# Kernel optimization log

Hardware: AMD Instinct MI355X
Metric: run time of the kernel (lower is better)

The kernel has to match this reference:

```python
import jax, jax.numpy as jnp
import numpy as np

B, T, D, H = 2, 2048, 2048, 16
HD = D // H
EPS = 1e-8
NEG = -1e9


def setup_inputs() -> dict:
    key = jax.random.key(0)
    ks = jax.random.split(key, 6)
    x = jax.random.normal(ks[0], (B, T, D), dtype=jnp.float32)
    # additive causal mask, broadcast over [B, H, T, T]
    causal = jnp.tril(jnp.ones((T, T), dtype=bool))
    attn_mask = jnp.where(causal, 0.0, NEG).astype(jnp.float32)[None, None]
    s = 1.0 / np.sqrt(D)
    w_norm = jnp.ones((D,), dtype=jnp.float32)
    wq = jax.random.normal(ks[1], (D, D), dtype=jnp.float32) * s
    wk = jax.random.normal(ks[2], (D, D), dtype=jnp.float32) * s
    wv = jax.random.normal(ks[3], (D, D), dtype=jnp.float32) * s
    wo = jax.random.normal(ks[4], (D, D), dtype=jnp.float32) * s
    return {"x": x, "attn_mask": attn_mask, "w_norm": w_norm,
            "wq": wq, "wk": wk, "wv": wv, "wo": wo}


def _rmsnorm(x, w):
    # norm = ||x||_2 * D^-0.5 ; out = w * x / (norm + eps)  (eps outside, as in source)
    norm = jnp.sqrt(jnp.sum(x * x, axis=-1, keepdims=True)) * (x.shape[-1] ** -0.5)
    return w * x / (norm + EPS)


def reference(x, attn_mask, w_norm, wq, wk, wv, wo):
    b, t, d = x.shape
    xn = _rmsnorm(x, w_norm)
    # Linear (no bias): y = x @ W^T ; split into heads -> [B, H, T, HD]
    def proj(w):
        return jnp.einsum('btd,ed->bte', xn, w).reshape(b, t, H, HD).transpose(0, 2, 1, 3)
    q, k, v = proj(wq), proj(wk), proj(wv)
    scale = HD ** -0.5
    w_scores = jnp.einsum('bhqd,bhkd->bhqk', q, k) * scale + attn_mask
    p = jax.nn.softmax(w_scores, axis=-1)
    out = jnp.einsum('bhqk,bhkd->bhqd', p, v)
    out = out.transpose(0, 2, 1, 3).reshape(b, t, d)
    return jnp.einsum('btd,ed->bte', out, wo)
```

## Files before the change

### kernel.cpp

```cpp
#include <hip/hip_runtime.h>
#include <stdint.h>

#define TT 2048
#define DD 2048
#define NHH 16
#define HDD 128
#define BTT 4096

typedef __attribute__((ext_vector_type(8))) short bf16x8;
typedef __attribute__((ext_vector_type(4))) float f32x4;

#define MF(a, b, c) __builtin_amdgcn_mfma_f32_16x16x32_bf16(a, b, c, 0, 0, 0)

__device__ __forceinline__ unsigned short f2bf(float f) {
    union { float f; uint32_t u; } v; v.f = f;
    uint32_t u = v.u;
    u += 0x7fffu + ((u >> 16) & 1u);
    return (unsigned short)(u >> 16);
}

__device__ __forceinline__ void gld16(const unsigned short* g, unsigned short* l) {
    __builtin_amdgcn_global_load_lds(
        (const __attribute__((address_space(1))) unsigned int*)g,
        (__attribute__((address_space(3))) unsigned int*)l, 16, 0, 0);
}

__global__ __launch_bounds__(256) void convert_w(const float* __restrict__ wq,
                                                 const float* __restrict__ wk,
                                                 const float* __restrict__ wv,
                                                 const float* __restrict__ wo,
                                                 unsigned short* __restrict__ out) {
    size_t gid = (size_t)blockIdx.x * 256 + threadIdx.x;
    size_t base = gid * 8;
    int which = (int)(base >> 22);
    const float* src = which == 0 ? wq : which == 1 ? wk : which == 2 ? wv : wo;
    size_t off = base & 4194303u;
    float4 a = ((const float4*)(src + off))[0];
    float4 b = ((const float4*)(src + off))[1];
    union { unsigned short us[8]; uint4 v; } pk;
    pk.us[0] = f2bf(a.x); pk.us[1] = f2bf(a.y); pk.us[2] = f2bf(a.z); pk.us[3] = f2bf(a.w);
    pk.us[4] = f2bf(b.x); pk.us[5] = f2bf(b.y); pk.us[6] = f2bf(b.z); pk.us[7] = f2bf(b.w);
    *(uint4*)(out + base) = pk.v;
}

__global__ __launch_bounds__(256) void rmsnorm_k(const float* __restrict__ x,
                                                 const float* __restrict__ w,
                                                 unsigned short* __restrict__ xn) {
    const int row = blockIdx.x;
    const int tid = threadIdx.x;
    const float* xr = x + (size_t)row * DD;
    float4 a = ((const float4*)xr)[tid * 2];
    float4 b = ((const float4*)xr)[tid * 2 + 1];
    float ss = a.x*a.x + a.y*a.y + a.z*a.z + a.w*a.w
             + b.x*b.x + b.y*b.y + b.z*b.z + b.w*b.w;
    #pragma unroll
    for (int m = 1; m < 64; m <<= 1) ss += __shfl_xor(ss, m, 64);
    __shared__ float wss[4];
    if ((tid & 63) == 0) wss[tid >> 6] = ss;
    __syncthreads();
    float total = wss[0] + wss[1] + wss[2] + wss[3];
    float norm = sqrtf(total) * 0.022097086912079612f;
    float inv = 1.0f / (norm + 1e-8f);
    float4 wa = ((const float4*)w)[tid * 2];
    float4 wb = ((const float4*)w)[tid * 2 + 1];
    union { unsigned short us[8]; uint4 v; } pk;
    pk.us[0] = f2bf(wa.x * a.x * inv); pk.us[1] = f2bf(wa.y * a.y * inv);
    pk.us[2] = f2bf(wa.z * a.z * inv); pk.us[3] = f2bf(wa.w * a.w * inv);
    pk.us[4] = f2bf(wb.x * b.x * inv); pk.us[5] = f2bf(wb.y * b.y * inv);
    pk.us[6] = f2bf(wb.z * b.z * inv); pk.us[7] = f2bf(wb.w * b.w * inv);
    ((uint4*)(xn + (size_t)row * DD))[tid] = pk.v;
}

__device__ __forceinline__ void gemm128x256_core(const unsigned short* __restrict__ Ag,
                                                 const unsigned short* __restrict__ Bg,
                                                 unsigned short* lds, f32x4 acc[4][4]) {
    const int tid = threadIdx.x;
    const int wave = tid >> 6, lane = tid & 63;
    const int wm = wave >> 2, wn = wave & 3;
    const int l15 = lane & 15, lq = lane >> 4;
    const unsigned short* ga  = Ag + (size_t)(wave * 16 + l15) * DD + lq * 8;
    const unsigned short* gb0 = Bg + (size_t)(wave * 32 + l15) * DD + lq * 8;
    const unsigned short* gb1 = Bg + (size_t)(wave * 32 + 16 + l15) * DD + lq * 8;
    const int da  = wave * 512 + lane * 8;
    const int db0 = 4096 + wave * 1024 + lane * 8;
    const int db1 = 4096 + wave * 1024 + 512 + lane * 8;
    const int ra = (wm * 4) * 512 + lq * 128 + l15 * 8;
    const int rb = 4096 + (wn * 4) * 512 + lq * 128 + l15 * 8;

    uint4 sA  = *(const uint4*)(ga);
    uint4 sB0 = *(const uint4*)(gb0);
    uint4 sB1 = *(const uint4*)(gb1);
    *(uint4*)(lds + da)  = sA;
    *(uint4*)(lds + db0) = sB0;
    *(uint4*)(lds + db1) = sB1;
    asm volatile("s_waitcnt lgkmcnt(0)" ::: "memory");
    __builtin_amdgcn_s_barrier();

    for (int kt = 0; kt < 64; kt++) {
        const int cur = (kt & 1) ? 12288 : 0;
        const int nxt = 12288 - cur;
        if (kt + 1 < 64) {
            const int ko = (kt + 1) * 32;
            sA  = *(const uint4*)(ga + ko);
            sB0 = *(const uint4*)(gb0 + ko);
            sB1 = *(const uint4*)(gb1 + ko);
            __builtin_amdgcn_sched_barrier(0);
        }
        const unsigned short* ac = lds + cur + ra;
        const unsigned short* bc = lds + cur + rb;
        bf16x8 a[4], b[4];
        #pragma unroll
        for (int i = 0; i < 4; i++) a[i] = *(const bf16x8*)(ac + i * 512);
        #pragma unroll
        for (int n = 0; n < 4; n++) b[n] = *(const bf16x8*)(bc + n * 512);
        asm volatile("s_waitcnt lgkmcnt(0)" ::: "memory");
        __builtin_amdgcn_sched_barrier(0);
        __builtin_amdgcn_s_setprio(1);
        #pragma unroll
        for (int i = 0; i < 4; i++)
            #pragma unroll
            for (int n = 0; n < 4; n++)
                acc[i][n] = MF(a[i], b[n], acc[i][n]);
        __builtin_amdgcn_s_setprio(0);
        if (kt + 1 < 64) {
            *(uint4*)(lds + nxt + da)  = sA;
            *(uint4*)(lds + nxt + db0) = sB0;
            *(uint4*)(lds + nxt + db1) = sB1;
            asm volatile("s_waitcnt lgkmcnt(0)" ::: "memory");
            __builtin_amdgcn_sched_barrier(0);
        }
        __builtin_amdgcn_s_barrier();
    }
}

__global__ __launch_bounds__(512, 4) void gemm_qkv(const unsigned short* __restrict__ A,
                                                   const unsigned short* __restrict__ W3,
                                                   unsigned short* __restrict__ O3) {
    __shared__ __align__(16) unsigned short lds[24576];
    const int orig = blockIdx.y * 32 + blockIdx.x;
    const int id = (orig & 7) * 96 + (orig >> 3);
    const int which = id >> 8;
    const int rem = id & 255;
    const int bn = rem >> 5, bm = rem & 31;
    const unsigned short* Bw = W3 + (size_t)which * DD * DD;
    unsigned short* C = O3 + (size_t)which * BTT * DD;
    const int m0 = bm * 128, n0 = bn * 256;
    const f32x4 zf = {0.f, 0.f, 0.f, 0.f};
    f32x4 acc[4][4];
    #pragma unroll
    for (int m = 0; m < 4; m++)
        #pragma unroll
        for (int n = 0; n < 4; n++) acc[m][n] = zf;
    gemm128x256_core(A + (size_t)m0 * DD, Bw + (size_t)n0 * DD, lds, acc);
    const int wave = threadIdx.x >> 6, lane = threadIdx.x & 63;
    const int wm = wave >> 2, wn = wave & 3;
    const int l15 = lane & 15, lq = lane >> 4;
    #pragma unroll
    for (int m = 0; m < 4; m++) {
        const int row = m0 + wm * 64 + m * 16 + lq * 4;
        #pragma unroll
        for (int n = 0; n < 4; n++) {
            const int col = n0 + wn * 64 + n * 16 + l15;
            #pragma unroll
            for (int r = 0; r < 4; r++)
                C[(size_t)(row + r) * DD + col] = f2bf(acc[m][n][r]);
        }
    }
}

__global__ __launch_bounds__(512, 4) void gemm_out(const unsigned short* __restrict__ A,
                                                   const unsigned short* __restrict__ Bw,
                                                   float* __restrict__ C) {
    __shared__ __align__(16) unsigned short lds[24576];
    const int orig = blockIdx.y * 32 + blockIdx.x;
    const int id = (orig & 7) * 32 + (orig >> 3);
    const int bn = id >> 5, bm = id & 31;
    const int m0 = bm * 128, n0 = bn * 256;
    const f32x4 zf = {0.f, 0.f, 0.f, 0.f};
    f32x4 acc[4][4];
    #pragma unroll
    for (int m = 0; m < 4; m++)
        #pragma unroll
        for (int n = 0; n < 4; n++) acc[m][n] = zf;
    gemm128x256_core(A + (size_t)m0 * DD, Bw + (size_t)n0 * DD, lds, acc);
    const int wave = threadIdx.x >> 6, lane = threadIdx.x & 63;
    const int wm = wave >> 2, wn = wave & 3;
    const int l15 = lane & 15, lq = lane >> 4;
    #pragma unroll
    for (int m = 0; m < 4; m++) {
        const int row = m0 + wm * 64 + m * 16 + lq * 4;
        #pragma unroll
        for (int n = 0; n < 4; n++) {
            const int col = n0 + wn * 64 + n * 16 + l15;
            #pragma unroll
            for (int r = 0; r < 4; r++)
                C[(size_t)(row + r) * DD + col] = acc[m][n][r];
        }
    }
}

__global__ __launch_bounds__(256) void attn_fused(const unsigned short* __restrict__ q,
                                                  const unsigned short* __restrict__ k,
                                                  const unsigned short* __restrict__ v,
                                                  unsigned short* __restrict__ o) {
    constexpr int LPP = 72;
    __shared__ __align__(16) unsigned short Ks[2][64 * 128];
    __shared__ __align__(16) unsigned short Vts[128 * 64];
    __shared__ __align__(16) unsigned short Ps[4 * 16 * LPP];
    const int lin = blockIdx.x + (blockIdx.y << 4) + (blockIdx.z << 8);
    const int slot = lin >> 3;
    const int g = ((lin & 7) << 2) + (slot >> 4);
    const int pairi = slot & 15;
    const int h = g & 15, b = g >> 4;
    const int tid = threadIdx.x, wave = tid >> 6, lane = tid & 63;
    const int l15 = lane & 15, lq = lane >> 4;
    const size_t rowbase = (size_t)b * TT;
    const int hcol = h * HDD;
    const float scale = 0.08838834764831845f;
    unsigned short* Pw = Ps + wave * 16 * LPP;
    const f32x4 zf = {0.f, 0.f, 0.f, 0.f};

    uint4 vr0, vr1, vr2, vr3;
    const int pr = tid >> 3;
    const int hc = (tid & 7) * 16;
    const int vsw0 = (2 * pr) ^ (((hc >> 3) & 7) << 3);
    const int vsw1 = (2 * pr) ^ ((((hc + 8) >> 3) & 7) << 3);

    const int klrow = lane >> 4;
    const int klch  = lane & 15;

    for (int half = 0; half < 2; half++) {
        const int qj = (half == 0) ? pairi : 31 - pairi;
        const int qt0 = qj * 64;
        bf16x8 aq[4];
        {
            const unsigned short* qrp = q + (rowbase + qt0 + wave * 16 + l15) * DD + hcol;
            #pragma unroll
            for (int kk = 0; kk < 4; kk++)
                aq[kk] = *(const bf16x8*)(qrp + kk * 32 + lq * 8);
        }
        f32x4 acc_o[8];
        #pragma unroll
        for (int jh = 0; jh < 8; jh++) acc_o[jh] = zf;
        float m_i[4], l_i[4];
        #pragma unroll
        for (int r = 0; r < 4; r++) { m_i[r] = -1e30f; l_i[r] = 0.f; }
        const int qp0 = qt0 + wave * 16 + lq * 4;
        const int nkt = qj + 1;

        __syncthreads();
        {
            const unsigned short* kg = k + rowbase * DD + hcol;
            const unsigned short* vg = v + rowbase * DD + hcol;
            #pragma unroll
            for (int i = 0; i < 4; i++) {
                const int r0 = wave * 16 + i * 4;
                const int row = r0 + klrow;
                const int gch = klch ^ (row & 7);
                gld16(kg + (size_t)row * DD + gch * 8, &Ks[0][r0 * 128]);
            }
            vr0 = *(const uint4*)(vg + (size_t)(2 * pr) * DD + hc);
            vr1 = *(const uint4*)(vg + (size_t)(2 * pr) * DD + hc + 8);
            vr2 = *(const uint4*)(vg + (size_t)(2 * pr + 1) * DD + hc);
            vr3 = *(const uint4*)(vg + (size_t)(2 * pr + 1) * DD + hc + 8);
        }

        for (int kt = 0; kt < nkt; kt++) {
            const int cur = kt & 1;
            __syncthreads();
            if (kt + 1 < nkt) {
                const unsigned short* kg = k + (rowbase + (kt + 1) * 64) * DD + hcol;
                #pragma unroll
                for (int i = 0; i < 4; i++) {
                    const int r0 = wave * 16 + i * 4;
                    const int row = r0 + klrow;
                    const int gch = klch ^ (row & 7);
                    gld16(kg + (size_t)row * DD + gch * 8, &Ks[cur ^ 1][r0 * 128]);
                }
            }
            {
                const unsigned short* s0 = (const unsigned short*)&vr0;
                const unsigned short* s1 = (const unsigned short*)&vr1;
                const unsigned short* s2 = (const unsigned short*)&vr2;
                const unsigned short* s3 = (const unsigned short*)&vr3;
                #pragma unroll
                for (int jj = 0; jj < 8; jj++) {
                    *(uint32_t*)(&Vts[(hc + jj) * 64 + vsw0]) =
                        (uint32_t)s0[jj] | ((uint32_t)s2[jj] << 16);
                    *(uint32_t*)(&Vts[(hc + 8 + jj) * 64 + vsw1]) =
                        (uint32_t)s1[jj] | ((uint32_t)s3[jj] << 16);
                }
            }
            if (kt + 1 < nkt) {
                const unsigned short* vg = v + (rowbase + (kt + 1) * 64) * DD + hcol;
                vr0 = *(const uint4*)(vg + (size_t)(2 * pr) * DD + hc);
                vr1 = *(const uint4*)(vg + (size_t)(2 * pr) * DD + hc + 8);
                vr2 = *(const uint4*)(vg + (size_t)(2 * pr + 1) * DD + hc);
                vr3 = *(const uint4*)(vg + (size_t)(2 * pr + 1) * DD + hc + 8);
            }
            const unsigned short* ksc = &Ks[cur][0];
            f32x4 accs[4];
            #pragma unroll
            for (int j = 0; j < 4; j++) accs[j] = zf;
            __builtin_amdgcn_s_setprio(1);
            #pragma unroll
            for (int j = 0; j < 4; j++)
                #pragma unroll
                for (int kk = 0; kk < 4; kk++) {
                    bf16x8 bk = *(const bf16x8*)(&ksc[(j * 16 + l15) * 128 +
                                                      (((kk * 4 + lq) ^ (l15 & 7)) * 8)]);
                    accs[j] = MF(aq[kk], bk, accs[j]);
                }
            __builtin_amdgcn_s_setprio(0);
            const int kbase = kt * 64;
            float rowmax[4] = {-1e30f, -1e30f, -1e30f, -1e30f};
            #pragma unroll
            for (int j = 0; j < 4; j++) {
                const int kp = kbase + j * 16 + l15;
                #pragma unroll
                for (int r = 0; r < 4; r++) {
                    float s = accs[j][r] * scale;
                    s = (kp > qp0 + r) ? -1e30f : s;
                    accs[j][r] = s;
                    rowmax[r] = fmaxf(rowmax[r], s);
                }
            }
            #pragma unroll
            for (int r = 0; r < 4; r++) {
                float mx = rowmax[r];
                mx = fmaxf(mx, __shfl_xor(mx, 1, 64));
                mx = fmaxf(mx, __shfl_xor(mx, 2, 64));
                mx = fmaxf(mx, __shfl_xor(mx, 4, 64));
                mx = fmaxf(mx, __shfl_xor(mx, 8, 64));
                float m_new = fmaxf(m_i[r], mx);
                float al = __expf(m_i[r] - m_new);
                m_i[r] = m_new;
                l_i[r] *= al;
                #pragma unroll
                for (int jh = 0; jh < 8; jh++) acc_o[jh][r] *= al;
            }
            float rowsum[4] = {0.f, 0.f, 0.f, 0.f};
            #pragma unroll
            for (int j = 0; j < 4; j++)
                #pragma unroll
                for (int r = 0; r < 4; r++) {
                    float p = __expf(accs[j][r] - m_i[r]);
                    rowsum[r] += p;
                    Pw[(lq * 4 + r) * LPP + j * 16 + l15] = f2bf(p);
                }
            #pragma unroll
            for (int r = 0; r < 4; r++) {
                float s = rowsum[r];
                s += __shfl_xor(s, 1, 64);
                s += __shfl_xor(s, 2, 64);
                s += __shfl_xor(s, 4, 64);
                s += __shfl_xor(s, 8, 64);
                l_i[r] += s;
            }
            __syncthreads();
            bf16x8 ap[2];
            #pragma unroll
            for (int kk = 0; kk < 2; kk++)
                ap[kk] = *(const bf16x8*)(&Pw[l15 * LPP + kk * 32 + lq * 8]);
            __builtin_amdgcn_s_setprio(1);
            #pragma unroll
            for (int jh = 0; jh < 8; jh++) {
                const int hd = jh * 16 + l15;
                const int vswz = ((hd >> 3) & 7) << 3;
                #pragma unroll
                for (int kk = 0; kk < 2; kk++) {
                    bf16x8 bv = *(const bf16x8*)(&Vts[hd * 64 + ((kk * 32 + lq * 8) ^ vswz)]);
                    acc_o[jh] = MF(ap[kk], bv, acc_o[jh]);
                }
            }
            __builtin_amdgcn_s_setprio(0);
        }
        #pragma unroll
        for (int jh = 0; jh < 8; jh++) {
            const int col = hcol + jh * 16 + l15;
            #pragma unroll
            for (int r = 0; r < 4; r++)
                o[(rowbase + qp0 + r) * DD + col] = f2bf(acc_o[jh][r] * (1.0f / l_i[r]));
        }
    }
}

extern "C" void kernel_launch(void* const* d_in, const int* in_sizes, int n_in,
                              void* d_out, int out_size, void* d_ws, size_t ws_size,
                              hipStream_t stream) {
    const float* x      = (const float*)d_in[0];
    const float* w_norm = (const float*)d_in[2];
    const float* wq     = (const float*)d_in[3];
    const float* wk     = (const float*)d_in[4];
    const float* wv     = (const float*)d_in[5];
    const float* wo     = (const float*)d_in[6];

    unsigned short* wbf = (unsigned short*)d_ws;
    unsigned short* xn  = wbf + (size_t)4 * DD * DD;
    unsigned short* qb  = xn + (size_t)BTT * DD;
    unsigned short* kb  = qb + (size_t)BTT * DD;
    unsigned short* vb  = kb + (size_t)BTT * DD;
    unsigned short* ab  = vb + (size_t)BTT * DD;

    convert_w<<<8192, 256, 0, stream>>>(wq, wk, wv, wo, wbf);
    rmsnorm_k<<<BTT, 256, 0, stream>>>(x, w_norm, xn);
    dim3 gqkv(32, 24);
    gemm_qkv<<<gqkv, 512, 0, stream>>>(xn, wbf, qb);
    dim3 gattn(16, NHH, 2);
    attn_fused<<<gattn, 256, 0, stream>>>(qb, kb, vb, ab);
    dim3 gout(32, 8);
    gemm_out<<<gout, 512, 0, stream>>>(ab, wbf + (size_t)3 * DD * DD, (float*)d_out);
}
```

Measured before the change: 479.3 us.

## Deepen GEMM global prefetch to two stages and simplify attention block mapping

The shared GEMM core now keeps two k-tiles of global loads in flight in two register sets, using explicit vmcnt waits before writing the older set to LDS. The goal is to hide more global-load latency behind the MFMA work. Launch bounds drop the min-blocks-per-CU hint of 4, giving the compiler more registers for the extra prefetch buffers at the possible cost of occupancy. The attention kernel also drops its XCD-aware block swizzle and maps blocks directly to (pair, head, batch), which may change L2 locality.

```diff
diff --git a/kernel.cpp b/kernel.cpp
--- a/kernel.cpp
+++ b/kernel.cpp
@@ -87,24 +87,30 @@
     const int ra = (wm * 4) * 512 + lq * 128 + l15 * 8;
     const int rb = 4096 + (wn * 4) * 512 + lq * 128 + l15 * 8;
 
-    uint4 sA  = *(const uint4*)(ga);
-    uint4 sB0 = *(const uint4*)(gb0);
-    uint4 sB1 = *(const uint4*)(gb1);
-    *(uint4*)(lds + da)  = sA;
-    *(uint4*)(lds + db0) = sB0;
-    *(uint4*)(lds + db1) = sB1;
+    uint4 pA, pB0, pB1, qA, qB0, qB1;
+
+    pA  = *(const uint4*)(ga);
+    pB0 = *(const uint4*)(gb0);
+    pB1 = *(const uint4*)(gb1);
+    asm volatile("s_waitcnt vmcnt(0)" ::: "memory");
+    *(uint4*)(lds + da)  = pA;
+    *(uint4*)(lds + db0) = pB0;
+    *(uint4*)(lds + db1) = pB1;
+    pA  = *(const uint4*)(ga + 32);
+    pB0 = *(const uint4*)(gb0 + 32);
+    pB1 = *(const uint4*)(gb1 + 32);
     asm volatile("s_waitcnt lgkmcnt(0)" ::: "memory");
     __builtin_amdgcn_s_barrier();
 
-    for (int kt = 0; kt < 64; kt++) {
-        const int cur = (kt & 1) ? 12288 : 0;
-        const int nxt = 12288 - cur;
-        if (kt + 1 < 64) {
-            const int ko = (kt + 1) * 32;
-            sA  = *(const uint4*)(ga + ko);
-            sB0 = *(const uint4*)(gb0 + ko);
-            sB1 = *(const uint4*)(gb1 + ko);
-            __builtin_amdgcn_sched_barrier(0);
+    auto body = [&](int kt, int cur, int nxt,
+                    uint4& cpA, uint4& cpB0, uint4& cpB1,
+                    uint4& cqA, uint4& cqB0, uint4& cqB1) {
+        const bool h2 = (kt + 2 < 64);
+        if (h2) {
+            const int ko = (kt + 2) * 32;
+            cqA  = *(const uint4*)(ga + ko);
+            cqB0 = *(const uint4*)(gb0 + ko);
+            cqB1 = *(const uint4*)(gb1 + ko);
         }
         const unsigned short* ac = lds + cur + ra;
         const unsigned short* bc = lds + cur + rb;
@@ -123,19 +129,27 @@
                 acc[i][n] = MF(a[i], b[n], acc[i][n]);
         __builtin_amdgcn_s_setprio(0);
         if (kt + 1 < 64) {
-            *(uint4*)(lds + nxt + da)  = sA;
-            *(uint4*)(lds + nxt + db0) = sB0;
-            *(uint4*)(lds + nxt + db1) = sB1;
+            if (h2) { asm volatile("s_waitcnt vmcnt(3)" ::: "memory"); }
+            else    { asm volatile("s_waitcnt vmcnt(0)" ::: "memory"); }
+            __builtin_amdgcn_sched_barrier(0);
+            *(uint4*)(lds + nxt + da)  = cpA;
+            *(uint4*)(lds + nxt + db0) = cpB0;
+            *(uint4*)(lds + nxt + db1) = cpB1;
             asm volatile("s_waitcnt lgkmcnt(0)" ::: "memory");
             __builtin_amdgcn_sched_barrier(0);
         }
         __builtin_amdgcn_s_barrier();
+    };
+
+    for (int k2 = 0; k2 < 32; k2++) {
+        body(2 * k2,     0,     12288, pA, pB0, pB1, qA, qB0, qB1);
+        body(2 * k2 + 1, 12288, 0,     qA, qB0, qB1, pA, pB0, pB1);
     }
 }
 
-__global__ __launch_bounds__(512, 4) void gemm_qkv(const unsigned short* __restrict__ A,
-                                                   const unsigned short* __restrict__ W3,
-                                                   unsigned short* __restrict__ O3) {
+__global__ __launch_bounds__(512) void gemm_qkv(const unsigned short* __restrict__ A,
+                                                const unsigned short* __restrict__ W3,
+                                                unsigned short* __restrict__ O3) {
     __shared__ __align__(16) unsigned short lds[24576];
     const int orig = blockIdx.y * 32 + blockIdx.x;
     const int id = (orig & 7) * 96 + (orig >> 3);
@@ -168,9 +182,9 @@
     }
 }
 
-__global__ __launch_bounds__(512, 4) void gemm_out(const unsigned short* __restrict__ A,
-                                                   const unsigned short* __restrict__ Bw,
-                                                   float* __restrict__ C) {
+__global__ __launch_bounds__(512) void gemm_out(const unsigned short* __restrict__ A,
+                                                const unsigned short* __restrict__ Bw,
+                                                float* __restrict__ C) {
     __shared__ __align__(16) unsigned short lds[24576];
     const int orig = blockIdx.y * 32 + blockIdx.x;
     const int id = (orig & 7) * 32 + (orig >> 3);
@@ -207,11 +221,7 @@
     __shared__ __align__(16) unsigned short Ks[2][64 * 128];
     __shared__ __align__(16) unsigned short Vts[128 * 64];
     __shared__ __align__(16) unsigned short Ps[4 * 16 * LPP];
-    const int lin = blockIdx.x + (blockIdx.y << 4) + (blockIdx.z << 8);
-    const int slot = lin >> 3;
-    const int g = ((lin & 7) << 2) + (slot >> 4);
-    const int pairi = slot & 15;
-    const int h = g & 15, b = g >> 4;
+    const int h = blockIdx.y, b = blockIdx.z;
     const int tid = threadIdx.x, wave = tid >> 6, lane = tid & 63;
     const int l15 = lane & 15, lq = lane >> 4;
     const size_t rowbase = (size_t)b * TT;
@@ -230,7 +240,7 @@
     const int klch  = lane & 15;
 
     for (int half = 0; half < 2; half++) {
-        const int qj = (half == 0) ? pairi : 31 - pairi;
+        const int qj = (half == 0) ? blockIdx.x : 31 - blockIdx.x;
         const int qt0 = qj * 64;
         bf16x8 aq[4];
         {
```

Result: faster. 455.9 us (-4.9%).
